# Kernel tuning notes

Measured on AMD Instinct MI355X. Metric: run time of the kernel, lower is better.

Reference implementation:

```python
import jax, jax.numpy as jnp
import numpy as np

T, N, I, H, OUT = 16, 4096, 4, 32, 1


def setup_inputs() -> dict:
    key = jax.random.key(0)
    ks = jax.random.split(key, 12)
    f32 = jnp.float32
    x_path = jax.random.normal(ks[0], (T, N, I), f32)
    adj = jax.random.normal(ks[1], (N, N), f32) / np.float32(np.sqrt(N))
    W_enc = jax.random.normal(ks[2], (I, H), f32) / np.float32(np.sqrt(I))
    b_enc = jnp.zeros((H,), f32)
    W_gcn = jax.random.normal(ks[3], (H, H), f32) / np.float32(np.sqrt(H))
    b_gcn = jnp.zeros((H,), f32)
    W_time = jax.random.normal(ks[4], (H, H), f32) / np.float32(np.sqrt(H))
    b_time = jnp.zeros((H,), f32)
    W_proj = jax.random.normal(ks[5], (H, H * I), f32) * np.float32(0.1 / np.sqrt(H))
    b_proj = jnp.zeros((H * I,), f32)
    W_d1 = jax.random.normal(ks[6], (H, 16), f32) / np.float32(np.sqrt(H))
    b_d1 = jnp.zeros((16,), f32)
    W_d2 = jax.random.normal(ks[7], (16, OUT), f32) / np.float32(4.0)
    b_d2 = jnp.zeros((OUT,), f32)
    return dict(x_path=x_path, adj=adj, W_enc=W_enc, b_enc=b_enc,
                W_gcn=W_gcn, b_gcn=b_gcn, W_time=W_time, b_time=b_time,
                W_proj=W_proj, b_proj=b_proj, W_d1=W_d1, b_d1=b_d1,
                W_d2=W_d2, b_d2=b_d2)


def _natural_cubic_coeffs(y):
    # y: (T, C) samples on uniform grid t=0..T-1 (h=1).
    # Natural cubic spline: tridiagonal solve for second derivatives M.
    Tn = y.shape[0]
    main = jnp.ones((Tn,), y.dtype).at[1:-1].set(4.0)
    A = jnp.diag(main)
    idx = jnp.arange(1, Tn - 1)
    A = A.at[idx, idx - 1].set(1.0).at[idx, idx + 1].set(1.0)
    rhs = jnp.zeros_like(y).at[1:-1].set(6.0 * (y[2:] - 2.0 * y[1:-1] + y[:-2]))
    M = jnp.linalg.solve(A, rhs)
    b = (y[1:] - y[:-1]) - (2.0 * M[:-1] + M[1:]) / 6.0
    c = M[:-1] / 2.0
    d = (M[1:] - M[:-1]) / 6.0
    return b, c, d  # each (T-1, C); dX/dt on interval i at local s: b+2cs+3ds^2


def reference(x_path, adj, W_enc, b_enc, W_gcn, b_gcn, W_time, b_time,
              W_proj, b_proj, W_d1, b_d1, W_d2, b_d2):
    Tn, Nn, In = x_path.shape
    Hn = W_enc.shape[1]
    y = x_path.reshape(Tn, Nn * In)
    sb, sc, sd = _natural_cubic_coeffs(y)

    # z0 = encoder(X(t0)); spline value at grid point 0 equals the sample.
    z0 = x_path[0] @ W_enc + b_enc  # (N, H)

    def vf(z, dxdt):
        # SpatialVectorField + projector + block-diagonal Jacobian applied to dX/dt.
        # z: (N, H), dxdt: (N, I)
        zn = adj @ z                                     # GCN neighbor aggregation
        h = jax.nn.relu(zn @ W_gcn + b_gcn + z @ W_time + b_time)
        sens = (h @ W_proj + b_proj).reshape(Nn, Hn, In)  # per-site Jacobian blocks
        # site_identity * sens -> block-diag; matmul with dX reduces to per-site contraction
        return jnp.einsum('nhi,ni->nh', sens, dxdt)

    def rk4_step(z, coefs):
        bi, ci, di = coefs  # (N*I,)
        def dxdt(s):
            return (bi + 2.0 * ci * s + 3.0 * di * s * s).reshape(Nn, In)
        k1 = vf(z, dxdt(0.0))
        k2 = vf(z + 0.5 * k1, dxdt(0.5))
        k3 = vf(z + 0.5 * k2, dxdt(0.5))
        k4 = vf(z + k3, dxdt(1.0))
        zn = z + (k1 + 2.0 * k2 + 2.0 * k3 + k4) / 6.0
        return zn, zn

    _, zs = jax.lax.scan(rk4_step, z0, (sb, sc, sd))
    zT = jnp.concatenate([z0[None], zs], axis=0)  # (T, N, H)

    hdec = jax.nn.relu(zT @ W_d1 + b_d1)
    return jax.nn.sigmoid(hdec @ W_d2 + b_d2)  # (T, N, OUT)
```

## Files before the change

### kernel.cpp

```cpp
#include <hip/hip_runtime.h>
#include <hip/hip_bf16.h>

#define NN 4096
#define NI 16384
#define HH 32

typedef __attribute__((ext_vector_type(8))) short short8;
typedef __attribute__((ext_vector_type(4))) float f32x4;
typedef unsigned long long u64;

union bfrag { short8 s8; u64 q[2]; };

__device__ __forceinline__ short f2bs(float f) {
  __hip_bfloat16 b = __float2bfloat16(f);
  return *(short*)&b;
}

__device__ __forceinline__ unsigned pack2(float lo, float hi) {
  return (unsigned)(unsigned short)f2bs(lo) |
         ((unsigned)(unsigned short)f2bs(hi) << 16);
}

__device__ __forceinline__ long zt_idx(int n, int h) {
  const int hb = h >> 4, hl = h & 15;
  const int kb = n >> 5, oct = (n >> 3) & 3, j = n & 7;
  return ((long)(hb * 128 + kb) * 64 + hl + 16 * oct) * 8 + j;
}

__global__ void k_spline(const float* __restrict__ x,
                         float* __restrict__ dx0, float* __restrict__ dxh,
                         float* __restrict__ dx1, unsigned* __restrict__ bar) {
  if (blockIdx.x == 0) {
    for (int i = threadIdx.x; i < 576; i += 256) bar[i] = 0u;
  }
  const int c = blockIdx.x * 256 + threadIdx.x;
  float y[16];
#pragma unroll
  for (int t = 0; t < 16; ++t) y[t] = x[t * NI + c];
  float cp[15], dp[15], M[16];
  cp[1] = 0.25f;
  dp[1] = (6.f * (y[2] - 2.f * y[1] + y[0])) * 0.25f;
#pragma unroll
  for (int i = 2; i <= 14; ++i) {
    float ri = 6.f * (y[i + 1] - 2.f * y[i] + y[i - 1]);
    float inv = 1.f / (4.f - cp[i - 1]);
    cp[i] = inv;
    dp[i] = (ri - dp[i - 1]) * inv;
  }
  M[0] = 0.f; M[15] = 0.f;
  M[14] = dp[14];
#pragma unroll
  for (int i = 13; i >= 1; --i) M[i] = dp[i] - cp[i] * M[i + 1];
#pragma unroll
  for (int i = 0; i < 15; ++i) {
    float b = (y[i + 1] - y[i]) - (2.f * M[i] + M[i + 1]) * (1.f / 6.f);
    float cc = 0.5f * M[i];
    float dd = (M[i + 1] - M[i]) * (1.f / 6.f);
    dx0[i * NI + c] = b;
    dxh[i * NI + c] = b + cc + 0.75f * dd;
    dx1[i * NI + c] = b + 2.f * cc + 3.f * dd;
  }
}

__device__ __forceinline__ void gridbar(unsigned* bar, int bid, int e) {
  __syncthreads();
  if (threadIdx.x == 0) {
    unsigned old = __hip_atomic_fetch_add(bar + (bid & 7) * 32, 1u,
                                          __ATOMIC_RELAXED, __HIP_MEMORY_SCOPE_AGENT);
    if (old == (unsigned)(32 * e - 1)) {
      unsigned rr = __hip_atomic_fetch_add(bar + 256, 1u,
                                           __ATOMIC_RELAXED, __HIP_MEMORY_SCOPE_AGENT);
      if (rr == (unsigned)(8 * e - 1)) {
#pragma unroll
        for (int g = 0; g < 8; ++g)
          __hip_atomic_store(bar + 320 + g * 32, (unsigned)e,
                             __ATOMIC_RELAXED, __HIP_MEMORY_SCOPE_AGENT);
      }
    }
    while (__hip_atomic_load(bar + 320 + (bid & 7) * 32, __ATOMIC_RELAXED,
                             __HIP_MEMORY_SCOPE_AGENT) < (unsigned)e)
      __builtin_amdgcn_s_sleep(2);
  }
  __syncthreads();
}

__device__ __forceinline__ void dec_block(const float* zsrc ,
                                          const float* Wd1s ,
                                          const float* dsm, float* op,
                                          int r0, int tid) {
  if (tid < 256) {
    const int rr = tid >> 4, jj = tid & 15;
    float hv = dsm[jj];
#pragma unroll
    for (int hh = 0; hh < 32; ++hh) hv = fmaf(zsrc[rr * 33 + hh], Wd1s[hh * 16 + jj], hv);
    float val = fmaxf(hv, 0.f) * dsm[16 + jj];
#pragma unroll
    for (int off = 1; off < 16; off <<= 1) val += __shfl_xor(val, off, 64);
    if (jj == 0)
      __hip_atomic_store(op + r0 + rr, 1.f / (1.f + expf(-(dsm[32] + val))),
                         __ATOMIC_RELAXED, __HIP_MEMORY_SCOPE_AGENT);
  }
}

__global__ __launch_bounds__(1024, 4) void k_ode(
    const float* __restrict__ adj, const float* __restrict__ x,
    const float* __restrict__ dx0, const float* __restrict__ dxh,
    const float* __restrict__ dx1,
    const float* __restrict__ We, const float* __restrict__ be,
    const float* __restrict__ Wg, const float* __restrict__ bg,
    const float* __restrict__ Wt, const float* __restrict__ bt,
    const float* __restrict__ Wp, const float* __restrict__ bp,
    const float* __restrict__ Wd1, const float* __restrict__ bd1,
    const float* __restrict__ Wd2, const float* __restrict__ bd2,
    short* __restrict__ zTa, short* __restrict__ zTb,
    unsigned* __restrict__ bar, float* __restrict__ out) {
  __shared__ float red2[16][34][17];
  __shared__ float zn_s[16][33];
  __shared__ float h_s[16][33];
  __shared__ float ze_s[16][33];
  __shared__ float zb_s[16][33];
  __shared__ float ka_s[16][33];
  __shared__ float Wg_s[32][32];
  __shared__ float Wt_s[32][32];
  __shared__ float Wp_s[32][136];
  __shared__ float Wd1_s[32][16];
  __shared__ float bgt_s[32];
  __shared__ float bp_s[128];
  __shared__ float dsm[33];

  const int tid = threadIdx.x;
  const int lane = tid & 63;
  const int w = tid >> 6;
  const int bid = blockIdx.x;
  const int r0 = bid * 16;
  const int fr = lane & 15, oct = lane >> 4;

  short8 av[8];
  {
    const float* arow = adj + (long)(r0 + fr) * NN + w * 256 + oct * 8;
#pragma unroll
    for (int i = 0; i < 8; ++i) {
      const float4 u0 = *(const float4*)(arow + i * 32);
      const float4 u1 = *(const float4*)(arow + i * 32 + 4);
      short8 rf;
      rf[0] = f2bs(u0.x); rf[1] = f2bs(u0.y); rf[2] = f2bs(u0.z); rf[3] = f2bs(u0.w);
      rf[4] = f2bs(u1.x); rf[5] = f2bs(u1.y); rf[6] = f2bs(u1.z); rf[7] = f2bs(u1.w);
      av[i] = rf;
    }
  }

  Wg_s[tid >> 5][tid & 31] = Wg[tid];
  Wt_s[tid >> 5][tid & 31] = Wt[tid];
#pragma unroll
  for (int idx = tid; idx < 4096; idx += 1024)
    Wp_s[idx >> 7][idx & 127] = Wp[idx];
  if (tid < 512) Wd1_s[tid >> 4][tid & 15] = Wd1[tid];
  if (tid < 32) bgt_s[tid] = bg[tid] + bt[tid];
  if (tid < 128) bp_s[tid] = bp[tid];
  if (tid < 16) { dsm[tid] = bd1[tid]; dsm[16 + tid] = Wd2[tid]; }
  if (tid == 0) dsm[32] = bd2[0];

  const int r = (tid >> 5) & 15, c = tid & 31;
  if (tid < 512) {
    const int n = r0 + r;
    float acc = be[c];
#pragma unroll
    for (int i = 0; i < 4; ++i) acc = fmaf(x[n * 4 + i], We[i * 32 + c], acc);
    zb_s[r][c] = acc;
    ze_s[r][c] = acc;
  }
  __syncthreads();
  if (tid >= 256 && tid < 384) {
    const int q = tid - 256;
    const int cc = q & 31, rr = (q >> 5) * 4;
    const u64 pk = (u64)pack2(ze_s[rr][cc], ze_s[rr + 1][cc]) |
                   ((u64)pack2(ze_s[rr + 2][cc], ze_s[rr + 3][cc]) << 32);
    __hip_atomic_store((u64*)zTa + (zt_idx(r0 + rr, cc) >> 2), pk,
                       __ATOMIC_RELAXED, __HIP_MEMORY_SCOPE_AGENT);
  }
  dec_block(&zb_s[0][0], &Wd1_s[0][0], dsm, out, r0, tid);

  int ep = 0;
  gridbar(bar, bid, ++ep);

  const short* zi = zTa;
  short* zo = zTb;

  for (int t = 0; t < 15; ++t) {
    const float* dt0 = dx0 + t * NI;
    const float* dth = dxh + t * NI;
    const float* dt1 = dx1 + t * NI;
    for (int j = 1; j <= 4; ++j) {
      const float* dxp = (j == 1) ? dt0 : (j == 4) ? dt1 : dth;

      float4 dxv;
      if (tid < 512) dxv = *(const float4*)(dxp + (long)(r0 + r) * 4);

      f32x4 a0 = {0.f, 0.f, 0.f, 0.f}, a1 = {0.f, 0.f, 0.f, 0.f};
      const u64* bq = (const u64*)zi + (size_t)w * 1024 + (lane << 1);
      bfrag bf[8];
#pragma unroll
      for (int i = 0; i < 8; ++i) {
        bf[i].q[0] = __hip_atomic_load(bq + i * 128,
                                       __ATOMIC_RELAXED, __HIP_MEMORY_SCOPE_AGENT);
        bf[i].q[1] = __hip_atomic_load(bq + i * 128 + 1,
                                       __ATOMIC_RELAXED, __HIP_MEMORY_SCOPE_AGENT);
      }
#pragma unroll
      for (int i = 0; i < 8; ++i)
        a0 = __builtin_amdgcn_mfma_f32_16x16x32_bf16(av[i], bf[i].s8, a0, 0, 0, 0);
#pragma unroll
      for (int i = 0; i < 8; ++i) {
        bf[i].q[0] = __hip_atomic_load(bq + 16384 + i * 128,
                                       __ATOMIC_RELAXED, __HIP_MEMORY_SCOPE_AGENT);
        bf[i].q[1] = __hip_atomic_load(bq + 16384 + i * 128 + 1,
                                       __ATOMIC_RELAXED, __HIP_MEMORY_SCOPE_AGENT);
      }
#pragma unroll
      for (int i = 0; i < 8; ++i)
        a1 = __builtin_amdgcn_mfma_f32_16x16x32_bf16(av[i], bf[i].s8, a1, 0, 0, 0);

      {
        const int crow = (lane >> 4) * 4, ccol = lane & 15;
#pragma unroll
        for (int q = 0; q < 4; ++q) {
          red2[crow + q][ccol][w] = a0[q];
          red2[crow + q][ccol + 16][w] = a1[q];
        }
      }
      __syncthreads();

      if (tid < 512) {
        float zn = 0.f;
#pragma unroll
        for (int q = 0; q < 16; ++q) zn += red2[r][c][q];
        zn_s[r][c] = zn;
      }
      __syncthreads();

      if (tid < 512) {
        float hv = bgt_s[c];
#pragma unroll
        for (int kk = 0; kk < 32; ++kk)
          hv = fmaf(zn_s[r][kk], Wg_s[kk][c], fmaf(ze_s[r][kk], Wt_s[kk][c], hv));
        h_s[r][c] = fmaxf(hv, 0.f);
      }
      __syncthreads();

      if (tid < 512) {
        float s0 = bp_s[c * 4], s1 = bp_s[c * 4 + 1];
        float s2 = bp_s[c * 4 + 2], s3 = bp_s[c * 4 + 3];
#pragma unroll
        for (int hp = 0; hp < 32; ++hp) {
          const float4 wv = *(const float4*)&Wp_s[hp][c * 4];
          const float hr = h_s[r][hp];
          s0 = fmaf(hr, wv.x, s0);
          s1 = fmaf(hr, wv.y, s1);
          s2 = fmaf(hr, wv.z, s2);
          s3 = fmaf(hr, wv.w, s3);
        }
        const float kv = s0 * dxv.x + s1 * dxv.y + s2 * dxv.z + s3 * dxv.w;
        float zev;
        if (j == 1)      { ka_s[r][c] = kv;            zev = zb_s[r][c] + 0.5f * kv; }
        else if (j == 2) { ka_s[r][c] += 2.f * kv;     zev = zb_s[r][c] + 0.5f * kv; }
        else if (j == 3) { ka_s[r][c] += 2.f * kv;     zev = zb_s[r][c] + kv; }
        else { zev = zb_s[r][c] + (ka_s[r][c] + kv) * (1.f / 6.f); zb_s[r][c] = zev; }
        ze_s[r][c] = zev;
      }
      __syncthreads();

      if (tid >= 256 && tid < 384) {
        const int q = tid - 256;
        const int cc = q & 31, rr = (q >> 5) * 4;
        const u64 pk = (u64)pack2(ze_s[rr][cc], ze_s[rr + 1][cc]) |
                       ((u64)pack2(ze_s[rr + 2][cc], ze_s[rr + 3][cc]) << 32);
        __hip_atomic_store((u64*)zo + (zt_idx(r0 + rr, cc) >> 2), pk,
                           __ATOMIC_RELAXED, __HIP_MEMORY_SCOPE_AGENT);
      }
      if (j == 4)
        dec_block(&zb_s[0][0], &Wd1_s[0][0], dsm, out + (t + 1) * NN, r0, tid);

      gridbar(bar, bid, ++ep);
      const short* tz = zi; zi = zo; zo = (short*)tz;
    }
  }
}

extern "C" void kernel_launch(void* const* d_in, const int* in_sizes, int n_in,
                              void* d_out, int out_size, void* d_ws, size_t ws_size,
                              hipStream_t stream) {
  (void)in_sizes; (void)n_in; (void)out_size; (void)ws_size;
  const float* x      = (const float*)d_in[0];
  const float* adj    = (const float*)d_in[1];
  const float* W_enc  = (const float*)d_in[2];
  const float* b_enc  = (const float*)d_in[3];
  const float* W_gcn  = (const float*)d_in[4];
  const float* b_gcn  = (const float*)d_in[5];
  const float* W_time = (const float*)d_in[6];
  const float* b_time = (const float*)d_in[7];
  const float* W_proj = (const float*)d_in[8];
  const float* b_proj = (const float*)d_in[9];
  const float* W_d1   = (const float*)d_in[10];
  const float* b_d1   = (const float*)d_in[11];
  const float* W_d2   = (const float*)d_in[12];
  const float* b_d2   = (const float*)d_in[13];
  float* out = (float*)d_out;

  float* dx0 = (float*)d_ws;
  float* dxh = dx0 + 15 * NI;
  float* dx1 = dxh + 15 * NI;
  short* zTa = (short*)(dx1 + 15 * NI);
  short* zTb = zTa + HH * NN;
  unsigned* bar = (unsigned*)(zTb + HH * NN);

  k_spline<<<64, 256, 0, stream>>>(x, dx0, dxh, dx1, bar);

  void* args[] = {(void*)&adj, (void*)&x, (void*)&dx0, (void*)&dxh, (void*)&dx1,
                  (void*)&W_enc, (void*)&b_enc, (void*)&W_gcn, (void*)&b_gcn,
                  (void*)&W_time, (void*)&b_time, (void*)&W_proj, (void*)&b_proj,
                  (void*)&W_d1, (void*)&b_d1, (void*)&W_d2, (void*)&b_d2,
                  (void*)&zTa, (void*)&zTb, (void*)&bar, (void*)&out};
  hipError_t err = hipLaunchCooperativeKernel((const void*)k_ode, dim3(256),
                                              dim3(1024), args, 0, stream);
  if (err != hipSuccess) {
    k_ode<<<256, 1024, 0, stream>>>(adj, x, dx0, dxh, dx1, W_enc, b_enc,
                                    W_gcn, b_gcn, W_time, b_time, W_proj, b_proj,
                                    W_d1, b_d1, W_d2, b_d2, zTa, zTb, bar, out);
  }
}
```

Before: 753.1 us.

## Halve block count to 128 with 32 rows per block and flat grid barrier

Each persistent block now owns 32 rows instead of 16. It keeps two 16-row adjacency tiles in registers and reuses every loaded z fragment for two MFMA accumulators. The grid barrier becomes a two-level counter: 16 groups of 8 blocks each bump a single global counter that all blocks spin on. The aim is to cut z reloads from L2, cut barrier participants, and let all 1024 threads do the elementwise stages. The costs are fewer CUs in use, more register pressure, and more serial per-block work.

```diff
diff --git a/kernel.cpp b/kernel.cpp
--- a/kernel.cpp
+++ b/kernel.cpp
@@ -4,6 +4,8 @@
 #define NN 4096
 #define NI 16384
 #define HH 32
+#define NBLK 128
+#define ROWS 32
 
 typedef __attribute__((ext_vector_type(8))) short short8;
 typedef __attribute__((ext_vector_type(4))) float f32x4;
@@ -65,20 +67,13 @@
 __device__ __forceinline__ void gridbar(unsigned* bar, int bid, int e) {
   __syncthreads();
   if (threadIdx.x == 0) {
-    unsigned old = __hip_atomic_fetch_add(bar + (bid & 7) * 32, 1u,
+    unsigned old = __hip_atomic_fetch_add(bar + (bid & 15) * 32, 1u,
                                           __ATOMIC_RELAXED, __HIP_MEMORY_SCOPE_AGENT);
-    if (old == (unsigned)(32 * e - 1)) {
-      unsigned rr = __hip_atomic_fetch_add(bar + 256, 1u,
-                                           __ATOMIC_RELAXED, __HIP_MEMORY_SCOPE_AGENT);
-      if (rr == (unsigned)(8 * e - 1)) {
-#pragma unroll
-        for (int g = 0; g < 8; ++g)
-          __hip_atomic_store(bar + 320 + g * 32, (unsigned)e,
+    if (old == (unsigned)(8 * e - 1))
+      __hip_atomic_fetch_add(bar + 512, 1u,
                              __ATOMIC_RELAXED, __HIP_MEMORY_SCOPE_AGENT);
-      }
-    }
-    while (__hip_atomic_load(bar + 320 + (bid & 7) * 32, __ATOMIC_RELAXED,
-                             __HIP_MEMORY_SCOPE_AGENT) < (unsigned)e)
+    while (__hip_atomic_load(bar + 512, __ATOMIC_RELAXED,
+                             __HIP_MEMORY_SCOPE_AGENT) < (unsigned)(16 * e))
       __builtin_amdgcn_s_sleep(2);
   }
   __syncthreads();
@@ -88,7 +83,7 @@
                                           const float* Wd1s ,
                                           const float* dsm, float* op,
                                           int r0, int tid) {
-  if (tid < 256) {
+  if (tid < 512) {
     const int rr = tid >> 4, jj = tid & 15;
     float hv = dsm[jj];
 #pragma unroll
@@ -114,12 +109,12 @@
     const float* __restrict__ Wd2, const float* __restrict__ bd2,
     short* __restrict__ zTa, short* __restrict__ zTb,
     unsigned* __restrict__ bar, float* __restrict__ out) {
-  __shared__ float red2[16][34][17];
-  __shared__ float zn_s[16][33];
-  __shared__ float h_s[16][33];
-  __shared__ float ze_s[16][33];
-  __shared__ float zb_s[16][33];
-  __shared__ float ka_s[16][33];
+  __shared__ float red2[32][33][17];
+  __shared__ float zn_s[32][33];
+  __shared__ float h_s[32][33];
+  __shared__ float ze_s[32][33];
+  __shared__ float zb_s[32][33];
+  __shared__ float ka_s[32][33];
   __shared__ float Wg_s[32][32];
   __shared__ float Wt_s[32][32];
   __shared__ float Wp_s[32][136];
@@ -132,12 +127,13 @@
   const int lane = tid & 63;
   const int w = tid >> 6;
   const int bid = blockIdx.x;
-  const int r0 = bid * 16;
+  const int r0 = bid * ROWS;
   const int fr = lane & 15, oct = lane >> 4;
 
-  short8 av[8];
-  {
-    const float* arow = adj + (long)(r0 + fr) * NN + w * 256 + oct * 8;
+  short8 av[16];
+#pragma unroll
+  for (int rt = 0; rt < 2; ++rt) {
+    const float* arow = adj + (long)(r0 + rt * 16 + fr) * NN + w * 256 + oct * 8;
 #pragma unroll
     for (int i = 0; i < 8; ++i) {
       const float4 u0 = *(const float4*)(arow + i * 32);
@@ -145,7 +141,7 @@
       short8 rf;
       rf[0] = f2bs(u0.x); rf[1] = f2bs(u0.y); rf[2] = f2bs(u0.z); rf[3] = f2bs(u0.w);
       rf[4] = f2bs(u1.x); rf[5] = f2bs(u1.y); rf[6] = f2bs(u1.z); rf[7] = f2bs(u1.w);
-      av[i] = rf;
+      av[rt * 8 + i] = rf;
     }
   }
 
@@ -160,8 +156,8 @@
   if (tid < 16) { dsm[tid] = bd1[tid]; dsm[16 + tid] = Wd2[tid]; }
   if (tid == 0) dsm[32] = bd2[0];
 
-  const int r = (tid >> 5) & 15, c = tid & 31;
-  if (tid < 512) {
+  const int r = tid >> 5, c = tid & 31;
+  {
     const int n = r0 + r;
     float acc = be[c];
 #pragma unroll
@@ -170,9 +166,8 @@
     ze_s[r][c] = acc;
   }
   __syncthreads();
-  if (tid >= 256 && tid < 384) {
-    const int q = tid - 256;
-    const int cc = q & 31, rr = (q >> 5) * 4;
+  if (tid < 256) {
+    const int cc = tid & 31, rr = (tid >> 5) * 4;
     const u64 pk = (u64)pack2(ze_s[rr][cc], ze_s[rr + 1][cc]) |
                    ((u64)pack2(ze_s[rr + 2][cc], ze_s[rr + 3][cc]) << 32);
     __hip_atomic_store((u64*)zTa + (zt_idx(r0 + rr, cc) >> 2), pk,
@@ -193,44 +188,50 @@
     for (int j = 1; j <= 4; ++j) {
       const float* dxp = (j == 1) ? dt0 : (j == 4) ? dt1 : dth;
 
-      float4 dxv;
-      if (tid < 512) dxv = *(const float4*)(dxp + (long)(r0 + r) * 4);
-
-      f32x4 a0 = {0.f, 0.f, 0.f, 0.f}, a1 = {0.f, 0.f, 0.f, 0.f};
-      const u64* bq = (const u64*)zi + (size_t)w * 1024 + (lane << 1);
-      bfrag bf[8];
-#pragma unroll
-      for (int i = 0; i < 8; ++i) {
-        bf[i].q[0] = __hip_atomic_load(bq + i * 128,
-                                       __ATOMIC_RELAXED, __HIP_MEMORY_SCOPE_AGENT);
-        bf[i].q[1] = __hip_atomic_load(bq + i * 128 + 1,
-                                       __ATOMIC_RELAXED, __HIP_MEMORY_SCOPE_AGENT);
-      }
-#pragma unroll
-      for (int i = 0; i < 8; ++i)
-        a0 = __builtin_amdgcn_mfma_f32_16x16x32_bf16(av[i], bf[i].s8, a0, 0, 0, 0);
-#pragma unroll
-      for (int i = 0; i < 8; ++i) {
-        bf[i].q[0] = __hip_atomic_load(bq + 16384 + i * 128,
-                                       __ATOMIC_RELAXED, __HIP_MEMORY_SCOPE_AGENT);
-        bf[i].q[1] = __hip_atomic_load(bq + 16384 + i * 128 + 1,
-                                       __ATOMIC_RELAXED, __HIP_MEMORY_SCOPE_AGENT);
-      }
-#pragma unroll
-      for (int i = 0; i < 8; ++i)
-        a1 = __builtin_amdgcn_mfma_f32_16x16x32_bf16(av[i], bf[i].s8, a1, 0, 0, 0);
-
+      const float4 dxv = *(const float4*)(dxp + (long)(r0 + r) * 4);
+
+      f32x4 a00 = {0.f,0.f,0.f,0.f}, a01 = {0.f,0.f,0.f,0.f};
+      f32x4 a10 = {0.f,0.f,0.f,0.f}, a11 = {0.f,0.f,0.f,0.f};
+      const u64* bq = (const u64*)zi + (size_t)(w * 8) * 128 + (lane << 1);
+      bfrag bf[4];
+#pragma unroll
+      for (int half = 0; half < 2; ++half) {
+        const u64* bh = bq + half * 16384;
+#pragma unroll
+        for (int batch = 0; batch < 2; ++batch) {
+#pragma unroll
+          for (int i = 0; i < 4; ++i) {
+            bf[i].q[0] = __hip_atomic_load(bh + (batch * 4 + i) * 128,
+                                           __ATOMIC_RELAXED, __HIP_MEMORY_SCOPE_AGENT);
+            bf[i].q[1] = __hip_atomic_load(bh + (batch * 4 + i) * 128 + 1,
+                                           __ATOMIC_RELAXED, __HIP_MEMORY_SCOPE_AGENT);
+          }
+#pragma unroll
+          for (int i = 0; i < 4; ++i) {
+            const int f = batch * 4 + i;
+            if (half == 0) {
+              a00 = __builtin_amdgcn_mfma_f32_16x16x32_bf16(av[f], bf[i].s8, a00, 0, 0, 0);
+              a10 = __builtin_amdgcn_mfma_f32_16x16x32_bf16(av[8 + f], bf[i].s8, a10, 0, 0, 0);
+            } else {
+              a01 = __builtin_amdgcn_mfma_f32_16x16x32_bf16(av[f], bf[i].s8, a01, 0, 0, 0);
+              a11 = __builtin_amdgcn_mfma_f32_16x16x32_bf16(av[8 + f], bf[i].s8, a11, 0, 0, 0);
+            }
+          }
+        }
+      }
       {
         const int crow = (lane >> 4) * 4, ccol = lane & 15;
 #pragma unroll
         for (int q = 0; q < 4; ++q) {
-          red2[crow + q][ccol][w] = a0[q];
-          red2[crow + q][ccol + 16][w] = a1[q];
+          red2[crow + q][ccol][w]            = a00[q];
+          red2[crow + q][ccol + 16][w]       = a01[q];
+          red2[16 + crow + q][ccol][w]       = a10[q];
+          red2[16 + crow + q][ccol + 16][w]  = a11[q];
         }
       }
       __syncthreads();
 
-      if (tid < 512) {
+      {
         float zn = 0.f;
 #pragma unroll
         for (int q = 0; q < 16; ++q) zn += red2[r][c][q];
@@ -238,7 +239,7 @@
       }
       __syncthreads();
 
-      if (tid < 512) {
+      {
         float hv = bgt_s[c];
 #pragma unroll
         for (int kk = 0; kk < 32; ++kk)
@@ -247,7 +248,7 @@
       }
       __syncthreads();
 
-      if (tid < 512) {
+      {
         float s0 = bp_s[c * 4], s1 = bp_s[c * 4 + 1];
         float s2 = bp_s[c * 4 + 2], s3 = bp_s[c * 4 + 3];
 #pragma unroll
@@ -269,9 +270,8 @@
       }
       __syncthreads();
 
-      if (tid >= 256 && tid < 384) {
-        const int q = tid - 256;
-        const int cc = q & 31, rr = (q >> 5) * 4;
+      if (tid < 256) {
+        const int cc = tid & 31, rr = (tid >> 5) * 4;
         const u64 pk = (u64)pack2(ze_s[rr][cc], ze_s[rr + 1][cc]) |
                        ((u64)pack2(ze_s[rr + 2][cc], ze_s[rr + 3][cc]) << 32);
         __hip_atomic_store((u64*)zo + (zt_idx(r0 + rr, cc) >> 2), pk,
@@ -320,11 +320,11 @@
                   (void*)&W_time, (void*)&b_time, (void*)&W_proj, (void*)&b_proj,
                   (void*)&W_d1, (void*)&b_d1, (void*)&W_d2, (void*)&b_d2,
                   (void*)&zTa, (void*)&zTb, (void*)&bar, (void*)&out};
-  hipError_t err = hipLaunchCooperativeKernel((const void*)k_ode, dim3(256),
+  hipError_t err = hipLaunchCooperativeKernel((const void*)k_ode, dim3(NBLK),
                                               dim3(1024), args, 0, stream);
   if (err != hipSuccess) {
-    k_ode<<<256, 1024, 0, stream>>>(adj, x, dx0, dxh, dx1, W_enc, b_enc,
-                                    W_gcn, b_gcn, W_time, b_time, W_proj, b_proj,
-                                    W_d1, b_d1, W_d2, b_d2, zTa, zTb, bar, out);
-  }
-}
+    k_ode<<<NBLK, 1024, 0, stream>>>(adj, x, dx0, dxh, dx1, W_enc, b_enc,
+                                     W_gcn, b_gcn, W_time, b_time, W_proj, b_proj,
+                                     W_d1, b_d1, W_d2, b_d2, zTa, zTb, bar, out);
+  }
+}
```

Result: slower. 901.9 us (+19.8%).

## Replace global grid barrier with per-wave dataflow counters on producer groups

Applied to the files above, without the earlier changes.

The full grid barrier after each RK stage is replaced by fine-grained counters. Each group of 16 blocks increments a counter once its bf16 z slice is stored, and each wave spins only on the counter for the 16 blocks whose z rows it consumes. This lets blocks proceed as soon as their inputs are ready instead of waiting for all blocks, which should cut barrier latency and skew. The z store now runs on one wave writing 8 rows per thread. The code also adds a fake data dependency on the polled counter to order the loads, and it relies on relaxed atomics together with a vmcnt wait for visibility.

```diff
diff --git a/kernel.cpp b/kernel.cpp
--- a/kernel.cpp
+++ b/kernel.cpp
@@ -60,28 +60,6 @@
     dxh[i * NI + c] = b + cc + 0.75f * dd;
     dx1[i * NI + c] = b + 2.f * cc + 3.f * dd;
   }
-}
-
-__device__ __forceinline__ void gridbar(unsigned* bar, int bid, int e) {
-  __syncthreads();
-  if (threadIdx.x == 0) {
-    unsigned old = __hip_atomic_fetch_add(bar + (bid & 7) * 32, 1u,
-                                          __ATOMIC_RELAXED, __HIP_MEMORY_SCOPE_AGENT);
-    if (old == (unsigned)(32 * e - 1)) {
-      unsigned rr = __hip_atomic_fetch_add(bar + 256, 1u,
-                                           __ATOMIC_RELAXED, __HIP_MEMORY_SCOPE_AGENT);
-      if (rr == (unsigned)(8 * e - 1)) {
-#pragma unroll
-        for (int g = 0; g < 8; ++g)
-          __hip_atomic_store(bar + 320 + g * 32, (unsigned)e,
-                             __ATOMIC_RELAXED, __HIP_MEMORY_SCOPE_AGENT);
-      }
-    }
-    while (__hip_atomic_load(bar + 320 + (bid & 7) * 32, __ATOMIC_RELAXED,
-                             __HIP_MEMORY_SCOPE_AGENT) < (unsigned)e)
-      __builtin_amdgcn_s_sleep(2);
-  }
-  __syncthreads();
 }
 
 __device__ __forceinline__ void dec_block(const float* zsrc ,
@@ -134,6 +112,8 @@
   const int bid = blockIdx.x;
   const int r0 = bid * 16;
   const int fr = lane & 15, oct = lane >> 4;
+  unsigned* cnt_mine = bar + (bid >> 4) * 32;
+  unsigned* cnt_wave = bar + w * 32;
 
   short8 av[8];
   {
@@ -170,119 +150,134 @@
     ze_s[r][c] = acc;
   }
   __syncthreads();
-  if (tid >= 256 && tid < 384) {
-    const int q = tid - 256;
-    const int cc = q & 31, rr = (q >> 5) * 4;
-    const u64 pk = (u64)pack2(ze_s[rr][cc], ze_s[rr + 1][cc]) |
-                   ((u64)pack2(ze_s[rr + 2][cc], ze_s[rr + 3][cc]) << 32);
-    __hip_atomic_store((u64*)zTa + (zt_idx(r0 + rr, cc) >> 2), pk,
+
+  if (w == 6) {
+    const int q = tid - 384, cc = q & 31, rr = (q >> 5) * 8;
+    const u64 pk0 = (u64)pack2(ze_s[rr][cc], ze_s[rr + 1][cc]) |
+                    ((u64)pack2(ze_s[rr + 2][cc], ze_s[rr + 3][cc]) << 32);
+    const u64 pk1 = (u64)pack2(ze_s[rr + 4][cc], ze_s[rr + 5][cc]) |
+                    ((u64)pack2(ze_s[rr + 6][cc], ze_s[rr + 7][cc]) << 32);
+    __hip_atomic_store((u64*)zTa + (zt_idx(r0 + rr, cc) >> 2), pk0,
                        __ATOMIC_RELAXED, __HIP_MEMORY_SCOPE_AGENT);
+    __hip_atomic_store((u64*)zTa + (zt_idx(r0 + rr + 4, cc) >> 2), pk1,
+                       __ATOMIC_RELAXED, __HIP_MEMORY_SCOPE_AGENT);
+    if (lane == 0) {
+      asm volatile("s_waitcnt vmcnt(0)" ::: "memory");
+      __hip_atomic_fetch_add(cnt_mine, 1u, __ATOMIC_RELAXED, __HIP_MEMORY_SCOPE_AGENT);
+    }
   }
   dec_block(&zb_s[0][0], &Wd1_s[0][0], dsm, out, r0, tid);
 
-  int ep = 0;
-  gridbar(bar, bid, ++ep);
-
-  const short* zi = zTa;
-  short* zo = zTb;
-
-  for (int t = 0; t < 15; ++t) {
-    const float* dt0 = dx0 + t * NI;
-    const float* dth = dxh + t * NI;
-    const float* dt1 = dx1 + t * NI;
-    for (int j = 1; j <= 4; ++j) {
-      const float* dxp = (j == 1) ? dt0 : (j == 4) ? dt1 : dth;
-
-      float4 dxv;
-      if (tid < 512) dxv = *(const float4*)(dxp + (long)(r0 + r) * 4);
-
-      f32x4 a0 = {0.f, 0.f, 0.f, 0.f}, a1 = {0.f, 0.f, 0.f, 0.f};
-      const u64* bq = (const u64*)zi + (size_t)w * 1024 + (lane << 1);
-      bfrag bf[8];
-#pragma unroll
-      for (int i = 0; i < 8; ++i) {
-        bf[i].q[0] = __hip_atomic_load(bq + i * 128,
-                                       __ATOMIC_RELAXED, __HIP_MEMORY_SCOPE_AGENT);
-        bf[i].q[1] = __hip_atomic_load(bq + i * 128 + 1,
-                                       __ATOMIC_RELAXED, __HIP_MEMORY_SCOPE_AGENT);
+  for (int e = 1; e <= 60; ++e) {
+    const int tt = (e - 1) >> 2, j = ((e - 1) & 3) + 1;
+    const float* dxp = (j == 1) ? dx0 + tt * NI
+                     : (j == 4) ? dx1 + tt * NI : dxh + tt * NI;
+    const short* zi = (e & 1) ? zTa : zTb;
+    short* zo = (e & 1) ? zTb : zTa;
+
+    float4 dxv;
+    if (tid < 512) dxv = *(const float4*)(dxp + (long)(r0 + r) * 4);
+
+    unsigned cv = 0;
+    if (lane == 0) {
+      cv = __hip_atomic_load(cnt_wave, __ATOMIC_RELAXED, __HIP_MEMORY_SCOPE_AGENT);
+      while (cv < (unsigned)(16 * e)) {
+        __builtin_amdgcn_s_sleep(1);
+        cv = __hip_atomic_load(cnt_wave, __ATOMIC_RELAXED, __HIP_MEMORY_SCOPE_AGENT);
       }
-#pragma unroll
-      for (int i = 0; i < 8; ++i)
-        a0 = __builtin_amdgcn_mfma_f32_16x16x32_bf16(av[i], bf[i].s8, a0, 0, 0, 0);
-#pragma unroll
-      for (int i = 0; i < 8; ++i) {
-        bf[i].q[0] = __hip_atomic_load(bq + 16384 + i * 128,
-                                       __ATOMIC_RELAXED, __HIP_MEMORY_SCOPE_AGENT);
-        bf[i].q[1] = __hip_atomic_load(bq + 16384 + i * 128 + 1,
-                                       __ATOMIC_RELAXED, __HIP_MEMORY_SCOPE_AGENT);
+    }
+    cv = (unsigned)__builtin_amdgcn_readfirstlane((int)cv);
+
+    f32x4 a0 = {0.f, 0.f, 0.f, 0.f}, a1 = {0.f, 0.f, 0.f, 0.f};
+    const u64* bq = (const u64*)zi + (size_t)w * 1024 + (lane << 1) + (cv >> 31);
+    bfrag bf[8];
+#pragma unroll
+    for (int i = 0; i < 8; ++i) {
+      bf[i].q[0] = __hip_atomic_load(bq + i * 128,
+                                     __ATOMIC_RELAXED, __HIP_MEMORY_SCOPE_AGENT);
+      bf[i].q[1] = __hip_atomic_load(bq + i * 128 + 1,
+                                     __ATOMIC_RELAXED, __HIP_MEMORY_SCOPE_AGENT);
+    }
+#pragma unroll
+    for (int i = 0; i < 8; ++i)
+      a0 = __builtin_amdgcn_mfma_f32_16x16x32_bf16(av[i], bf[i].s8, a0, 0, 0, 0);
+#pragma unroll
+    for (int i = 0; i < 8; ++i) {
+      bf[i].q[0] = __hip_atomic_load(bq + 16384 + i * 128,
+                                     __ATOMIC_RELAXED, __HIP_MEMORY_SCOPE_AGENT);
+      bf[i].q[1] = __hip_atomic_load(bq + 16384 + i * 128 + 1,
+                                     __ATOMIC_RELAXED, __HIP_MEMORY_SCOPE_AGENT);
+    }
+#pragma unroll
+    for (int i = 0; i < 8; ++i)
+      a1 = __builtin_amdgcn_mfma_f32_16x16x32_bf16(av[i], bf[i].s8, a1, 0, 0, 0);
+
+    {
+      const int crow = (lane >> 4) * 4, ccol = lane & 15;
+#pragma unroll
+      for (int q = 0; q < 4; ++q) {
+        red2[crow + q][ccol][w] = a0[q];
+        red2[crow + q][ccol + 16][w] = a1[q];
       }
-#pragma unroll
-      for (int i = 0; i < 8; ++i)
-        a1 = __builtin_amdgcn_mfma_f32_16x16x32_bf16(av[i], bf[i].s8, a1, 0, 0, 0);
-
-      {
-        const int crow = (lane >> 4) * 4, ccol = lane & 15;
-#pragma unroll
-        for (int q = 0; q < 4; ++q) {
-          red2[crow + q][ccol][w] = a0[q];
-          red2[crow + q][ccol + 16][w] = a1[q];
-        }
+    }
+    __syncthreads();
+
+    if (tid < 512) {
+      float zn = 0.f;
+#pragma unroll
+      for (int q = 0; q < 16; ++q) zn += red2[r][c][q];
+      zn_s[r][c] = zn;
+    }
+    __syncthreads();
+
+    if (tid < 512) {
+      float hv = bgt_s[c];
+#pragma unroll
+      for (int kk = 0; kk < 32; ++kk)
+        hv = fmaf(zn_s[r][kk], Wg_s[kk][c], fmaf(ze_s[r][kk], Wt_s[kk][c], hv));
+      h_s[r][c] = fmaxf(hv, 0.f);
+    }
+    __syncthreads();
+
+    if (tid < 512) {
+      float s0 = bp_s[c * 4], s1 = bp_s[c * 4 + 1];
+      float s2 = bp_s[c * 4 + 2], s3 = bp_s[c * 4 + 3];
+#pragma unroll
+      for (int hp = 0; hp < 32; ++hp) {
+        const float4 wv = *(const float4*)&Wp_s[hp][c * 4];
+        const float hr = h_s[r][hp];
+        s0 = fmaf(hr, wv.x, s0);
+        s1 = fmaf(hr, wv.y, s1);
+        s2 = fmaf(hr, wv.z, s2);
+        s3 = fmaf(hr, wv.w, s3);
       }
-      __syncthreads();
-
-      if (tid < 512) {
-        float zn = 0.f;
-#pragma unroll
-        for (int q = 0; q < 16; ++q) zn += red2[r][c][q];
-        zn_s[r][c] = zn;
+      const float kv = s0 * dxv.x + s1 * dxv.y + s2 * dxv.z + s3 * dxv.w;
+      float zev;
+      if (j == 1)      { ka_s[r][c] = kv;            zev = zb_s[r][c] + 0.5f * kv; }
+      else if (j == 2) { ka_s[r][c] += 2.f * kv;     zev = zb_s[r][c] + 0.5f * kv; }
+      else if (j == 3) { ka_s[r][c] += 2.f * kv;     zev = zb_s[r][c] + kv; }
+      else { zev = zb_s[r][c] + (ka_s[r][c] + kv) * (1.f / 6.f); zb_s[r][c] = zev; }
+      ze_s[r][c] = zev;
+    }
+    __syncthreads();
+
+    if (w == 6) {
+      const int q = tid - 384, cc = q & 31, rr = (q >> 5) * 8;
+      const u64 pk0 = (u64)pack2(ze_s[rr][cc], ze_s[rr + 1][cc]) |
+                      ((u64)pack2(ze_s[rr + 2][cc], ze_s[rr + 3][cc]) << 32);
+      const u64 pk1 = (u64)pack2(ze_s[rr + 4][cc], ze_s[rr + 5][cc]) |
+                      ((u64)pack2(ze_s[rr + 6][cc], ze_s[rr + 7][cc]) << 32);
+      __hip_atomic_store((u64*)zo + (zt_idx(r0 + rr, cc) >> 2), pk0,
+                         __ATOMIC_RELAXED, __HIP_MEMORY_SCOPE_AGENT);
+      __hip_atomic_store((u64*)zo + (zt_idx(r0 + rr + 4, cc) >> 2), pk1,
+                         __ATOMIC_RELAXED, __HIP_MEMORY_SCOPE_AGENT);
+      if (lane == 0) {
+        asm volatile("s_waitcnt vmcnt(0)" ::: "memory");
+        __hip_atomic_fetch_add(cnt_mine, 1u, __ATOMIC_RELAXED, __HIP_MEMORY_SCOPE_AGENT);
       }
-      __syncthreads();
-
-      if (tid < 512) {
-        float hv = bgt_s[c];
-#pragma unroll
-        for (int kk = 0; kk < 32; ++kk)
-          hv = fmaf(zn_s[r][kk], Wg_s[kk][c], fmaf(ze_s[r][kk], Wt_s[kk][c], hv));
-        h_s[r][c] = fmaxf(hv, 0.f);
-      }
-      __syncthreads();
-
-      if (tid < 512) {
-        float s0 = bp_s[c * 4], s1 = bp_s[c * 4 + 1];
-        float s2 = bp_s[c * 4 + 2], s3 = bp_s[c * 4 + 3];
-#pragma unroll
-        for (int hp = 0; hp < 32; ++hp) {
-          const float4 wv = *(const float4*)&Wp_s[hp][c * 4];
-          const float hr = h_s[r][hp];
-          s0 = fmaf(hr, wv.x, s0);
-          s1 = fmaf(hr, wv.y, s1);
-          s2 = fmaf(hr, wv.z, s2);
-          s3 = fmaf(hr, wv.w, s3);
-        }
-        const float kv = s0 * dxv.x + s1 * dxv.y + s2 * dxv.z + s3 * dxv.w;
-        float zev;
-        if (j == 1)      { ka_s[r][c] = kv;            zev = zb_s[r][c] + 0.5f * kv; }
-        else if (j == 2) { ka_s[r][c] += 2.f * kv;     zev = zb_s[r][c] + 0.5f * kv; }
-        else if (j == 3) { ka_s[r][c] += 2.f * kv;     zev = zb_s[r][c] + kv; }
-        else { zev = zb_s[r][c] + (ka_s[r][c] + kv) * (1.f / 6.f); zb_s[r][c] = zev; }
-        ze_s[r][c] = zev;
-      }
-      __syncthreads();
-
-      if (tid >= 256 && tid < 384) {
-        const int q = tid - 256;
-        const int cc = q & 31, rr = (q >> 5) * 4;
-        const u64 pk = (u64)pack2(ze_s[rr][cc], ze_s[rr + 1][cc]) |
-                       ((u64)pack2(ze_s[rr + 2][cc], ze_s[rr + 3][cc]) << 32);
-        __hip_atomic_store((u64*)zo + (zt_idx(r0 + rr, cc) >> 2), pk,
-                           __ATOMIC_RELAXED, __HIP_MEMORY_SCOPE_AGENT);
-      }
-      if (j == 4)
-        dec_block(&zb_s[0][0], &Wd1_s[0][0], dsm, out + (t + 1) * NN, r0, tid);
-
-      gridbar(bar, bid, ++ep);
-      const short* tz = zi; zi = zo; zo = (short*)tz;
-    }
+    }
+    if (j == 4)
+      dec_block(&zb_s[0][0], &Wd1_s[0][0], dsm, out + (tt + 1) * NN, r0, tid);
   }
 }
 
```

Result: slower. 784.9 us (+4.2%).
